# Performance work log

Measured on AMD Instinct MI355X. Metric: run time of the kernel, lower is better.

Reference implementation:

```python
import jax, jax.numpy as jnp
import numpy as np

B, S, D, H = 4, 1024, 1024, 16
HD = D // H          # head space dim = 64
FF = 4 * D           # ffn hidden = 4096
EPS = 1e-6

# ---- Lorentz manifold helpers (curvature k=1: -t^2 + |s|^2 = -1) ----

def to_manifold(space):
    t = jnp.sqrt(jnp.sum(space * space, -1, keepdims=True) + 1.0)
    return jnp.concatenate([t, space], -1)

def l_inner(x, y):
    return -x[..., 0] * y[..., 0] + jnp.sum(x[..., 1:] * y[..., 1:], -1)

def project(z):
    # renormalize onto hyperboloid: z / sqrt(|<z,z>_L|)   (Lorentz midpoint / LResNet)
    d = jnp.sqrt(jnp.clip(-l_inner(z, z), EPS))
    return z / d[..., None]

def hyp_layernorm(x, g, b):
    s = x[..., 1:]
    mu = jnp.mean(s, -1, keepdims=True)
    var = jnp.var(s, -1, keepdims=True)
    s = (s - mu) * jax.lax.rsqrt(var + 1e-5) * g + b
    return to_manifold(s)

def apply_rope(xs, cos, sin):
    # xs [B,S,H,HD]; cos/sin [S,HD//2]; freqs broadcast as [1,S,1,HD//2]
    x2 = xs.reshape(*xs.shape[:-1], HD // 2, 2)
    c = cos[None, :, None, :]
    s = sin[None, :, None, :]
    xr = x2[..., 0] * c - x2[..., 1] * s
    xi = x2[..., 0] * s + x2[..., 1] * c
    return jnp.stack([xr, xi], -1).reshape(xs.shape)


def setup_inputs() -> dict:
    key = jax.random.key(0)
    ks = jax.random.split(key, 8)
    def w(k, shape, fan_in):
        return jax.random.normal(k, shape, jnp.float32) / np.sqrt(fan_in).astype(np.float32)
    x = to_manifold(0.5 * jax.random.normal(ks[0], (B, S, D), jnp.float32))
    pos = jnp.arange(S, dtype=jnp.float32)[:, None]
    inv = 1.0 / (10000.0 ** (jnp.arange(0, HD, 2, dtype=jnp.float32) / HD))
    ang = pos * inv[None, :]
    return {
        'x': x,
        'rope_cos': jnp.cos(ang), 'rope_sin': jnp.sin(ang),
        'norm1_g': jnp.ones((D,), jnp.float32), 'norm1_b': jnp.zeros((D,), jnp.float32),
        'Wq': w(ks[1], (H, D + 1, HD), D + 1), 'bq': jnp.zeros((H, HD), jnp.float32),
        'Wk': w(ks[2], (H, D + 1, HD), D + 1), 'bk': jnp.zeros((H, HD), jnp.float32),
        'Wv': w(ks[3], (H, D + 1, HD), D + 1), 'bv': jnp.zeros((H, HD), jnp.float32),
        'attn_scale': jnp.asarray(np.sqrt(HD), jnp.float32),
        'attn_bias': jnp.zeros((), jnp.float32),
        'Wo': w(ks[4], (H * (HD + 1), D), H * (HD + 1)), 'bo': jnp.zeros((D,), jnp.float32),
        'w_res1': jnp.asarray(1.0, jnp.float32),
        'norm2_g': jnp.ones((D,), jnp.float32), 'norm2_b': jnp.zeros((D,), jnp.float32),
        'W1': w(ks[5], (D + 1, FF), D + 1), 'b1': jnp.zeros((FF,), jnp.float32),
        'W2': w(ks[6], (FF + 1, D), FF + 1), 'b2': jnp.zeros((D,), jnp.float32),
        'w_res2': jnp.asarray(1.0, jnp.float32),
    }


def reference(x, rope_cos, rope_sin, norm1_g, norm1_b, Wq, bq, Wk, bk, Wv, bv,
              attn_scale, attn_bias, Wo, bo, w_res1, norm2_g, norm2_b,
              W1, b1, W2, b2, w_res2):
    # ---- pre-norm ----
    xn = hyp_layernorm(x, norm1_g, norm1_b)
    # ---- per-head Lorentz linear (space part), inline RoPE on q/k ----
    qs = jnp.einsum('bsd,hde->bshe', xn, Wq) + bq          # [B,S,H,HD]
    ksp = jnp.einsum('bsd,hde->bshe', xn, Wk) + bk
    vsp = jnp.einsum('bsd,hde->bshe', xn, Wv) + bv
    qs = apply_rope(qs, rope_cos, rope_sin)
    ksp = apply_rope(ksp, rope_cos, rope_sin)
    # hyperbolic normalization of q/k: unit space norm, time recomputed
    qs = qs * jax.lax.rsqrt(jnp.sum(qs * qs, -1, keepdims=True) + EPS)
    ksp = ksp * jax.lax.rsqrt(jnp.sum(ksp * ksp, -1, keepdims=True) + EPS)
    q = to_manifold(qs)                                    # [B,S,H,HD+1]
    k = to_manifold(ksp)
    v = to_manifold(vsp)
    # ---- curvature-aware scores: 2 + 2 <q,k>_L (neg sq Lorentz distance) ----
    sgn = jnp.concatenate([-jnp.ones((1,), q.dtype), jnp.ones((HD,), q.dtype)])
    cin = jnp.einsum('bshe,bthe->bhst', q * sgn, k)        # Minkowski inner [B,H,S,S]
    att = (2.0 + 2.0 * cin) / attn_scale + attn_bias
    P = jax.nn.softmax(att, axis=-1)
    # ---- Lorentz midpoint aggregation of values ----
    m = jnp.einsum('bhst,bthe->bshe', P, v)
    m = project(m)                                         # back onto hyperboloid
    # ---- heads concat + output Lorentz linear ----
    cat = m.reshape(B, S, H * (HD + 1))
    attn_out = to_manifold(cat @ Wo + bo)
    # ---- LResNet residual 1 ----
    x = project(x + w_res1 * attn_out)
    # ---- Lorentz FFN ----
    h = hyp_layernorm(x, norm2_g, norm2_b)
    h = to_manifold(jax.nn.gelu(h @ W1 + b1))
    mlp = to_manifold(h @ W2 + b2)
    # ---- LResNet residual 2 ----
    x = project(x + w_res2 * mlp)
    return x
```

## Files before the change

### kernel.cpp

```cpp
#include <hip/hip_runtime.h>
#include <hip/hip_bf16.h>

typedef __hip_bfloat16 bf16;
typedef __attribute__((ext_vector_type(8))) short short8;
typedef __attribute__((ext_vector_type(4))) float f32x4;

#define B_  4
#define S_  1024
#define H_  16
#define R_  4096
#define LD_ 1088

#define MBL 1048576L
#define OFF_WQKVT (0L)
#define OFF_WOT   (6684672L)
#define OFF_X2    (0L)
#define OFF_W1T   (9L*MBL)
#define OFF_W2T   (18L*MBL)
#define OFF_BIAS  (26L*MBL)
#define OFF_XNB   (27L*MBL + MBL/2)
#define OFF_MCAT  OFF_XNB
#define OFF_HBUF  OFF_XNB
#define OFF_QPS   (36L*MBL)
#define OFF_ARAW  OFF_QPS
#define OFF_KPS   (44L*MBL)
#define OFF_VT    (52L*MBL)
#define OFF_QT    (62L*MBL)
#define OFF_KT    (62L*MBL + 262144L)
#define OFF_HHBIG (44L*MBL)
#define OFF_MLPB  (76L*MBL)
#define OFF_HHC   (36L*MBL)
#define OFF_MLPF  (44L*MBL)
#define BQKV 0
#define BOF  16384
#define B1F  32768
#define B2F  65536
#define W2R0 81920
#define RCF  98304
#define RSNF 262144
#define SCLF 409600
#define TACC 425984
#define FLAG 458752

__device__ __forceinline__ bf16  f2bf(float v) { return __float2bfloat16(v); }
__device__ __forceinline__ float bf2f(bf16 v)  { return __bfloat162float(v); }
__device__ __forceinline__ unsigned short bf2s(float v) {
  return __builtin_bit_cast(unsigned short, __float2bfloat16(v));
}
__device__ __forceinline__ float ldu(const void* p, long i, int isbf) {
  return isbf ? bf2f(((const bf16*)p)[i]) : ((const float*)p)[i];
}
__device__ __forceinline__ void stu(void* p, long i, float v, int isbf) {
  if (isbf) ((bf16*)p)[i] = f2bf(v);
  else      ((float*)p)[i] = v;
}
__device__ __forceinline__ float gelu_f(float v) {
  const float u = 0.7978845608028654f * (v + 0.044715f * v * v * v);
  const float e = __expf(fminf(2.f * u, 80.f));
  return 0.5f * v * (1.f + (e - 1.f) / (e + 1.f));
}
__device__ __forceinline__ float bfu_lo(unsigned u) {
  return __builtin_bit_cast(float, u << 16);
}
__device__ __forceinline__ float bfu_hi(unsigned u) {
  return __builtin_bit_cast(float, u & 0xFFFF0000u);
}

__device__ __forceinline__ void gload16(const bf16* g, short* l) {
  __builtin_amdgcn_global_load_lds(
      (const __attribute__((address_space(1))) unsigned int*)g,
      (__attribute__((address_space(3))) unsigned int*)l, 16, 0, 0);
}

__global__ void detect_kernel(const unsigned* __restrict__ g, int* __restrict__ flag) {
  if (threadIdx.x == 0) flag[0] = (g[0] == 0x3F803F80u) ? 1 : 0;
}

__global__ __launch_bounds__(256) void zero16_kernel(uint4* __restrict__ p, int n16) {
  int i = blockIdx.x * 256 + threadIdx.x;
  if (i < n16) p[i] = uint4{0, 0, 0, 0};
}

__device__ __forceinline__ float bred_f(float v, float* sh) {
#pragma unroll
  for (int o = 32; o; o >>= 1) v += __shfl_xor(v, o);
  __syncthreads();
  if ((threadIdx.x & 63) == 0) sh[threadIdx.x >> 6] = v;
  __syncthreads();
  return sh[0] + sh[1] + sh[2] + sh[3];
}
__device__ __forceinline__ double bred_d(double v, double* sh) {
#pragma unroll
  for (int o = 32; o; o >>= 1) v += __shfl_xor(v, o);
  __syncthreads();
  if ((threadIdx.x & 63) == 0) sh[threadIdx.x >> 6] = v;
  __syncthreads();
  return sh[0] + sh[1] + sh[2] + sh[3];
}

__global__ __launch_bounds__(256) void mega_prep(
    const void* x, const void* rc, const void* rsn, const void* n1g, const void* n1b,
    const void* Wq, const void* bq, const void* Wk, const void* bk,
    const void* Wv, const void* bv, const void* scl, const void* ab,
    const void* Wo, const void* bo, const void* wr1,
    const void* W1, const void* b1, const void* W2, const void* b2, const void* wr2,
    char* bias_base, bf16* __restrict__ wqkvT, bf16* __restrict__ woT,
    bf16* __restrict__ w1T, bf16* __restrict__ w2T, bf16* __restrict__ xnb,
    const int* __restrict__ flag) {
  const int isbf = flag[0];
  __shared__ float tl[64][65];
  const int tid = threadIdx.x;
  int bid = blockIdx.x;
  if (bid < 297) {
    int i = bid * 256 + tid;
    float* bqkvf = (float*)(bias_base + BQKV);
    if (i < 1024)        { bqkvf[i] = ldu(bq, i, isbf); return; }
    if (i < 2048)        { bqkvf[i] = ldu(bk, i - 1024, isbf); return; }
    if (i < 3072)        { bqkvf[i] = ldu(bv, i - 2048, isbf); return; }
    if (i < 4096)        { ((float*)(bias_base + BOF))[i - 3072] = ldu(bo, i - 3072, isbf); return; }
    if (i < 8192)        { ((float*)(bias_base + B1F))[i - 4096] = ldu(b1, i - 4096, isbf); return; }
    if (i < 9216)        { ((float*)(bias_base + B2F))[i - 8192] = ldu(b2, i - 8192, isbf); return; }
    if (i < 10240)       { ((float*)(bias_base + W2R0))[i - 9216] = ldu(W2, i - 9216, isbf); return; }
    if (i < 10240+32768) { ((float*)(bias_base + RCF))[i - 10240] = ldu(rc, i - 10240, isbf); return; }
    if (i < 10240+65536) { ((float*)(bias_base + RSNF))[i - 43008] = ldu(rsn, i - 43008, isbf); return; }
    if (i == 75776)      { ((float*)(bias_base + SCLF))[0] = ldu(scl, 0, isbf); return; }
    if (i == 75777)      { ((float*)(bias_base + SCLF))[1] = ldu(ab, 0, isbf); return; }
    if (i == 75778)      { ((float*)(bias_base + SCLF))[2] = ldu(wr1, 0, isbf); return; }
    if (i == 75779)      { ((float*)(bias_base + SCLF))[3] = ldu(wr2, 0, isbf); return; }
    return;
  }
  bid -= 297;
  const int tx = tid & 63, tg = tid >> 6;
  if (bid < 816) {
    int k0 = (bid % 17) * 64, z = bid / 17;
    int mode = z >> 4, h = z & 15;
    const void* src = (mode == 0) ? Wq : (mode == 1) ? Wk : Wv;
    const long soff = (long)h * 1025 * 64;
    int base_n = mode * 1024 + h * 64;
    for (int i = tg; i < 64; i += 4) {
      int k = k0 + i;
      tl[i][tx] = (k < 1025) ? ldu(src, soff + (long)k * 64 + tx, isbf) : 0.f;
    }
    __syncthreads();
    for (int i = tg; i < 64; i += 4) {
      int k = k0 + tx;
      if (k < LD_) wqkvT[(long)(base_n + i) * LD_ + k] = f2bf(tl[tx][i]);
    }
    return;
  }
  bid -= 816;
  if (bid < 272) {
    int k0 = (bid % 17) * 64, n0 = (bid / 17) * 64;
    for (int i = tg; i < 64; i += 4) {
      int kp = k0 + i;
      float v = 0.f;
      if (kp < 1056) {
        int h = kp / 66, e = kp - h * 66;
        if (e < 65) v = ldu(Wo, (long)(h * 65 + e) * 1024 + n0 + tx, isbf);
      }
      tl[i][tx] = v;
    }
    __syncthreads();
    for (int i = tg; i < 64; i += 4) {
      int kp = k0 + tx;
      if (kp < LD_) woT[(long)(n0 + i) * LD_ + kp] = f2bf(tl[tx][i]);
    }
    return;
  }
  bid -= 272;
  if (bid < 1088) {
    int k0 = (bid % 17) * 64, n0 = (bid / 17) * 64;
    for (int i = tg; i < 64; i += 4) {
      int k = k0 + i;
      tl[i][tx] = (k < 1025) ? ldu(W1, (long)k * 4096 + n0 + tx, isbf) : 0.f;
    }
    __syncthreads();
    for (int i = tg; i < 64; i += 4) {
      int k = k0 + tx;
      if (k < LD_) w1T[(long)(n0 + i) * LD_ + k] = f2bf(tl[tx][i]);
    }
    return;
  }
  bid -= 1088;
  if (bid < 1024) {
    int k0 = (bid % 64) * 64, n0 = (bid / 64) * 64;
    for (int i = tg; i < 64; i += 4) {
      int k = k0 + i;
      tl[i][tx] = ldu(W2, 1024 + (long)k * 1024 + n0 + tx, isbf);
    }
    __syncthreads();
    for (int i = tg; i < 64; i += 4) {
      int k = k0 + tx;
      w2T[(long)(n0 + i) * 4096 + k] = f2bf(tl[tx][i]);
    }
    return;
  }
  bid -= 1024;
  {
    float* red = &tl[0][0];
    const long base = (long)bid * 1025;
    const long obase = (long)bid * LD_;
    float v[4];
#pragma unroll
    for (int i = 0; i < 4; i++) v[i] = ldu(x, base + 1 + tid * 4 + i, isbf);
    float s = 0.f, s2 = 0.f;
#pragma unroll
    for (int i = 0; i < 4; i++) { s += v[i]; s2 += v[i] * v[i]; }
    s  = bred_f(s,  red);
    s2 = bred_f(s2, red);
    const float mu  = s * (1.f / 1024.f);
    const float var = s2 * (1.f / 1024.f) - mu * mu;
    const float rs  = rsqrtf(var + 1e-5f);
    float n[4], ns = 0.f;
#pragma unroll
    for (int i = 0; i < 4; i++) {
      const int e = tid * 4 + i;
      n[i] = (v[i] - mu) * rs * ldu(n1g, e, isbf) + ldu(n1b, e, isbf);
      ns += n[i] * n[i];
    }
    ns = bred_f(ns, red);
    if (tid == 0) xnb[obase] = f2bf(sqrtf(ns + 1.f));
#pragma unroll
    for (int i = 0; i < 4; i++) xnb[obase + 1 + tid * 4 + i] = f2bf(n[i]);
    if (tid < 63) xnb[obase + 1025 + tid] = f2bf(0.f);
  }
}

template <int EPI, bool SS>
__global__ __launch_bounds__(256) void mfma_gemm(const bf16* __restrict__ A, int lda,
                                                 const bf16* __restrict__ Bw, int ldb, int K,
                                                 const float* __restrict__ bias,
                                                 void* __restrict__ Cv, int ldc, int accf,
                                                 float* __restrict__ tacc) {
  __shared__ __align__(16) short As[2][128 * 32];
  __shared__ __align__(16) short Bs[2][64 * 32];
  const int tid = threadIdx.x, lane = tid & 63, wv = tid >> 6;
  const int quad = lane >> 4, q15 = lane & 15;
  const int wave_m = wv & 1, wave_n = wv >> 1;
  const int n0 = blockIdx.x * 64, m0 = blockIdx.y * 128;
  const int sa0 = wv * 128 + lane, sa1 = sa0 + 64;
  const int ra0 = sa0 >> 2, ca0 = (sa0 & 3) ^ (ra0 & 3);
  const int ra1 = sa1 >> 2, ca1 = (sa1 & 3) ^ (ra1 & 3);
  const int rb = tid >> 2, cb = (tid & 3) ^ (rb & 3);
  const int kswz = (quad ^ (q15 & 3)) * 8;
  const bf16* pa0 = A + (long)(m0 + ra0) * lda + ca0 * 8;
  const bf16* pa1 = A + (long)(m0 + ra1) * lda + ca1 * 8;
  const bf16* pb  = Bw + (long)(n0 + rb) * ldb + cb * 8;
  f32x4 acc[4][2] = {};
  for (int k0 = 0; k0 < K; k0 += 64) {
#pragma unroll
    for (int p = 0; p < 2; p++) {
      gload16(pa0 + p * 32, As[p] + sa0 * 8);
      gload16(pa1 + p * 32, As[p] + sa1 * 8);
      gload16(pb + p * 32, Bs[p] + tid * 8);
    }
    pa0 += 64; pa1 += 64; pb += 64;
    __syncthreads();
#pragma unroll
    for (int p = 0; p < 2; p++) {
      short8 af[4], bfr[2];
#pragma unroll
      for (int i = 0; i < 4; i++)
        af[i] = *(const short8*)(As[p] + (wave_m * 64 + i * 16 + q15) * 32 + kswz);
#pragma unroll
      for (int i = 0; i < 2; i++)
        bfr[i] = *(const short8*)(Bs[p] + (wave_n * 32 + i * 16 + q15) * 32 + kswz);
#pragma unroll
      for (int mi = 0; mi < 4; mi++)
#pragma unroll
        for (int ni = 0; ni < 2; ni++)
          acc[mi][ni] = __builtin_amdgcn_mfma_f32_16x16x32_bf16(af[mi], bfr[ni], acc[mi][ni], 0, 0, 0);
    }
    __syncthreads();
  }
#pragma unroll
  for (int mi = 0; mi < 4; mi++) {
#pragma unroll
    for (int r = 0; r < 4; r++) {
      const int m = m0 + wave_m * 64 + mi * 16 + quad * 4 + r;
      float s2 = 0.f;
#pragma unroll
      for (int ni = 0; ni < 2; ni++) {
        const int n = n0 + wave_n * 32 + ni * 16 + q15;
        float v = acc[mi][ni][r] + (bias ? bias[n] : 0.f);
        const long idx = (long)m * ldc + n;
        if (EPI == 0) {
          float* Cf = (float*)Cv;
          if (accf) v += Cf[idx];
          Cf[idx] = v;
        } else if (EPI == 1) {
          ((bf16*)Cv)[idx] = f2bf(v);
        } else {
          v = gelu_f(v);
          ((bf16*)Cv)[idx] = f2bf(v);
        }
        if (SS) s2 += v * v;
      }
      if (SS) {
        s2 += __shfl_xor(s2, 1);
        s2 += __shfl_xor(s2, 2);
        s2 += __shfl_xor(s2, 4);
        s2 += __shfl_xor(s2, 8);
        if (q15 == 0) atomicAdd(tacc + m, s2);
      }
    }
  }
}

template <int EPI>
__global__ __launch_bounds__(256) void mfma_gemm128(const bf16* __restrict__ A, int lda,
                                                    const bf16* __restrict__ Bw, int ldb, int K,
                                                    const float* __restrict__ bias,
                                                    void* __restrict__ Cv, int ldc, int accf) {
  __shared__ __align__(16) short As[2][128 * 32];
  __shared__ __align__(16) short Bs[2][128 * 32];
  const int tid = threadIdx.x, lane = tid & 63, wv = tid >> 6;
  const int quad = lane >> 4, q15 = lane & 15;
  const int wave_m = wv & 1, wave_n = wv >> 1;
  const int n0 = blockIdx.x * 128, m0 = blockIdx.y * 128;
  const int s0 = wv * 128 + lane, s1 = s0 + 64;
  const int r0 = s0 >> 2, c0 = (s0 & 3) ^ (r0 & 3);
  const int r1 = s1 >> 2, c1 = (s1 & 3) ^ (r1 & 3);
  const int kswz = (quad ^ (q15 & 3)) * 8;
  const bf16* pa0 = A + (long)(m0 + r0) * lda + c0 * 8;
  const bf16* pa1 = A + (long)(m0 + r1) * lda + c1 * 8;
  const bf16* pb0 = Bw + (long)(n0 + r0) * ldb + c0 * 8;
  const bf16* pb1 = Bw + (long)(n0 + r1) * ldb + c1 * 8;
  f32x4 acc[4][4] = {};
  for (int k0 = 0; k0 < K; k0 += 64) {
#pragma unroll
    for (int p = 0; p < 2; p++) {
      gload16(pa0 + p * 32, As[p] + s0 * 8);
      gload16(pa1 + p * 32, As[p] + s1 * 8);
      gload16(pb0 + p * 32, Bs[p] + s0 * 8);
      gload16(pb1 + p * 32, Bs[p] + s1 * 8);
    }
    pa0 += 64; pa1 += 64; pb0 += 64; pb1 += 64;
    __syncthreads();
#pragma unroll
    for (int p = 0; p < 2; p++) {
      short8 af[4], bfr[4];
#pragma unroll
      for (int i = 0; i < 4; i++) {
        af[i]  = *(const short8*)(As[p] + (wave_m * 64 + i * 16 + q15) * 32 + kswz);
        bfr[i] = *(const short8*)(Bs[p] + (wave_n * 64 + i * 16 + q15) * 32 + kswz);
      }
#pragma unroll
      for (int mi = 0; mi < 4; mi++)
#pragma unroll
        for (int ni = 0; ni < 4; ni++)
          acc[mi][ni] = __builtin_amdgcn_mfma_f32_16x16x32_bf16(af[mi], bfr[ni], acc[mi][ni], 0, 0, 0);
    }
    __syncthreads();
  }
#pragma unroll
  for (int mi = 0; mi < 4; mi++) {
#pragma unroll
    for (int r = 0; r < 4; r++) {
      const int m = m0 + wave_m * 64 + mi * 16 + quad * 4 + r;
#pragma unroll
      for (int ni = 0; ni < 4; ni++) {
        const int n = n0 + wave_n * 64 + ni * 16 + q15;
        float v = acc[mi][ni][r] + (bias ? bias[n] : 0.f);
        const long idx = (long)m * ldc + n;
        if (EPI == 0) {
          float* Cf = (float*)Cv;
          if (accf) v += Cf[idx];
          Cf[idx] = v;
        } else if (EPI == 1) {
          ((bf16*)Cv)[idx] = f2bf(v);
        } else {
          ((bf16*)Cv)[idx] = f2bf(gelu_f(v));
        }
      }
    }
  }
}

__global__ __launch_bounds__(256) void gemm_qkv(const bf16* __restrict__ A,
                                                const bf16* __restrict__ Wt,
                                                const char* __restrict__ bias_base,
                                                bf16* __restrict__ qPs, float* __restrict__ qtc,
                                                bf16* __restrict__ kPs, float* __restrict__ ktc,
                                                bf16* __restrict__ vT) {
  __shared__ __align__(16) short As[2][128 * 32];
  __shared__ __align__(16) short Bs[2][128 * 32];
  const int tid = threadIdx.x, lane = tid & 63, wv = tid >> 6;
  const int quad = lane >> 4, q15 = lane & 15;
  const int wave_m = wv & 1, wave_n = wv >> 1;
  const int n0 = blockIdx.x * 128, m0 = blockIdx.y * 128;
  const int s0 = wv * 128 + lane, s1 = s0 + 64;
  const int r0 = s0 >> 2, c0 = (s0 & 3) ^ (r0 & 3);
  const int r1 = s1 >> 2, c1 = (s1 & 3) ^ (r1 & 3);
  const int kswz = (quad ^ (q15 & 3)) * 8;
  const float* bqkvf = (const float*)(bias_base + BQKV);
  const float* rcf   = (const float*)(bias_base + RCF);
  const float* rsnf  = (const float*)(bias_base + RSNF);
  const bf16* pa0 = A + (long)(m0 + r0) * LD_ + c0 * 8;
  const bf16* pa1 = A + (long)(m0 + r1) * LD_ + c1 * 8;
  const bf16* pb0 = Wt + (long)(n0 + r0) * LD_ + c0 * 8;
  const bf16* pb1 = Wt + (long)(n0 + r1) * LD_ + c1 * 8;
  f32x4 acc[4][4] = {};
  for (int k0 = 0; k0 < LD_; k0 += 64) {
#pragma unroll
    for (int p = 0; p < 2; p++) {
      gload16(pa0 + p * 32, As[p] + s0 * 8);
      gload16(pa1 + p * 32, As[p] + s1 * 8);
      gload16(pb0 + p * 32, Bs[p] + s0 * 8);
      gload16(pb1 + p * 32, Bs[p] + s1 * 8);
    }
    pa0 += 64; pa1 += 64; pb0 += 64; pb1 += 64;
    __syncthreads();
#pragma unroll
    for (int p = 0; p < 2; p++) {
      short8 af[4], bfr[4];
#pragma unroll
      for (int i = 0; i < 4; i++) {
        af[i]  = *(const short8*)(As[p] + (wave_m * 64 + i * 16 + q15) * 32 + kswz);
        bfr[i] = *(const short8*)(Bs[p] + (wave_n * 64 + i * 16 + q15) * 32 + kswz);
      }
#pragma unroll
      for (int mi = 0; mi < 4; mi++)
#pragma unroll
        for (int ni = 0; ni < 4; ni++)
          acc[mi][ni] = __builtin_amdgcn_mfma_f32_16x16x32_bf16(af[mi], bfr[ni], acc[mi][ni], 0, 0, 0);
    }
    __syncthreads();
  }
  const int hg = (n0 >> 6) + wave_n;
  const int mode = hg >> 4, h = hg & 15;
  const int nb = hg * 64;
#pragma unroll
  for (int mi = 0; mi < 4; mi++) {
#pragma unroll
    for (int r = 0; r < 4; r++) {
      const int m = m0 + wave_m * 64 + mi * 16 + quad * 4 + r;
      const int bb = m >> 10, s = m & 1023;
      const int bh = bb * H_ + h;
      float v[4];
#pragma unroll
      for (int ns = 0; ns < 4; ns++) v[ns] = acc[mi][ns][r] + bqkvf[nb + ns * 16 + q15];
      if (mode < 2) {
#pragma unroll
        for (int ns = 0; ns < 4; ns++) {
          const int eg = ns * 16 + q15;
          const int j = eg >> 1;
          const float c = rcf[s * 32 + j], sn = rsnf[s * 32 + j];
          const float p = __shfl_xor(v[ns], 1);
          v[ns] = ((eg & 1) == 0) ? (v[ns] * c - p * sn) : (p * sn + v[ns] * c);
        }
      }
      float ss = v[0] * v[0] + v[1] * v[1] + v[2] * v[2] + v[3] * v[3];
#pragma unroll
      for (int o = 8; o; o >>= 1) ss += __shfl_xor(ss, o);
      if (mode == 0) {
        const float sc = rsqrtf(ss + 1e-6f);
        const long rb2 = (long)(bh * 1024 + s) * 64;
#pragma unroll
        for (int ns = 0; ns < 4; ns++) qPs[rb2 + ns * 16 + q15] = f2bf(v[ns] * sc);
        if (q15 == 0) qtc[bh * 1024 + s] = sqrtf(ss / (ss + 1e-6f) + 1.f);
      } else if (mode == 1) {
        const float sc = rsqrtf(ss + 1e-6f);
        const long rb2 = (long)(bh * 1024 + s) * 64;
#pragma unroll
        for (int ns = 0; ns < 4; ns++) kPs[rb2 + ns * 16 + q15] = f2bf(v[ns] * sc);
        if (q15 == 0) ktc[bh * 1024 + s] = sqrtf(ss / (ss + 1e-6f) + 1.f);
      } else {
        const long vb = (long)bh * 81920;
#pragma unroll
        for (int ns = 0; ns < 4; ns++) vT[vb + (long)(1 + ns * 16 + q15) * 1024 + s] = f2bf(v[ns]);
        if (q15 == 0) vT[vb + s] = f2bf(sqrtf(ss + 1.f));
      }
    }
  }
}

__global__ __launch_bounds__(256) void attn_kernel(const bf16* __restrict__ qPs,
                                                   const float* __restrict__ qtc,
                                                   const bf16* __restrict__ kPs,
                                                   const float* __restrict__ ktc,
                                                   const bf16* __restrict__ vT,
                                                   const float* __restrict__ scalf,
                                                   bf16* __restrict__ mcat) {
  __shared__ __align__(16) short kbuf[64 * 72];
  __shared__ __align__(16) short vbuf[80 * 72];
  __shared__ __align__(16) short pbuf[64 * 72];
  __shared__ float tkl[64];
  const int tid = threadIdx.x, lane = tid & 63, wv = tid >> 6;
  const int quad = lane >> 4, q15 = lane & 15;
  const int id = blockIdx.x;
  const int cxd = id & 7, jj_ = id >> 3;
  const int bh = cxd * 8 + (jj_ & 7), qt_ = jj_ >> 3;
  const float inv_scale = 1.f / scalf[0];
  const long qrow = (long)(bh * 1024 + qt_ * 64 + wv * 16 + q15) * 64;
  const short8 aq0 = *(const short8*)(qPs + qrow + quad * 8);
  const short8 aq1 = *(const short8*)(qPs + qrow + 32 + quad * 8);
  float tqr[4];
#pragma unroll
  for (int r = 0; r < 4; r++) tqr[r] = qtc[bh * 1024 + qt_ * 64 + wv * 16 + quad * 4 + r];
  f32x4 out[5];
#pragma unroll
  for (int mt = 0; mt < 5; mt++) out[mt] = f32x4{0, 0, 0, 0};
  float lip[4] = {0.f, 0.f, 0.f, 0.f};
  const int srcl = (q15 >> 2) << 4;
  for (int kt = 0; kt < 16; kt++) {
    __syncthreads();
#pragma unroll
    for (int c = 0; c < 2; c++) {
      const int id2 = c * 256 + tid, row = id2 >> 3, off = id2 & 7;
      *(uint4*)(kbuf + row * 72 + off * 8) =
          *(const uint4*)(kPs + (long)(bh * 1024 + kt * 64 + row) * 64 + off * 8);
    }
#pragma unroll
    for (int c = 0; c < 3; c++) {
      const int id2 = c * 256 + tid;
      if (id2 < 640) {
        const int row = id2 >> 3, off = id2 & 7;
        *(uint4*)(vbuf + row * 72 + off * 8) =
            *(const uint4*)(vT + (long)bh * 81920 + (long)row * 1024 + kt * 64 + off * 8);
      }
    }
    if (tid < 64) tkl[tid] = ktc[bh * 1024 + kt * 64 + tid];
    __syncthreads();
    f32x4 sacc[4] = {f32x4{0,0,0,0}, f32x4{0,0,0,0}, f32x4{0,0,0,0}, f32x4{0,0,0,0}};
#pragma unroll
    for (int ns = 0; ns < 4; ns++) {
      short8 b0 = *(const short8*)(kbuf + (ns * 16 + q15) * 72 + quad * 8);
      short8 b1 = *(const short8*)(kbuf + (ns * 16 + q15) * 72 + 32 + quad * 8);
      sacc[ns] = __builtin_amdgcn_mfma_f32_16x16x32_bf16(aq0, b0, sacc[ns], 0, 0, 0);
      sacc[ns] = __builtin_amdgcn_mfma_f32_16x16x32_bf16(aq1, b1, sacc[ns], 0, 0, 0);
    }
#pragma unroll
    for (int ns = 0; ns < 4; ns++) {
      const float tk = tkl[ns * 16 + q15];
#pragma unroll
      for (int r = 0; r < 4; r++) {
        const float pv = __expf((2.f + 2.f * (sacc[ns][r] - tqr[r] * tk)) * inv_scale);
        lip[r] += pv;
        pbuf[(wv * 16 + quad * 4 + r) * 72 + ns * 16 + q15] = (short)bf2s(pv);
      }
    }
#pragma unroll
    for (int mt = 0; mt < 5; mt++)
#pragma unroll
      for (int kc = 0; kc < 2; kc++) {
        short8 av = *(const short8*)(vbuf + (mt * 16 + q15) * 72 + kc * 32 + quad * 8);
        short8 bp = *(const short8*)(pbuf + (wv * 16 + q15) * 72 + kc * 32 + quad * 8);
        out[mt] = __builtin_amdgcn_mfma_f32_16x16x32_bf16(av, bp, out[mt], 0, 0, 0);
      }
  }
  {
#pragma unroll
    for (int o = 8; o; o >>= 1)
#pragma unroll
      for (int r = 0; r < 4; r++) lip[r] += __shfl_xor(lip[r], o);
    float linv[4];
#pragma unroll
    for (int r = 0; r < 4; r++) linv[r] = 1.f / lip[r];
    const float t0 = __shfl(linv[0], srcl), t1 = __shfl(linv[1], srcl);
    const float t2 = __shfl(linv[2], srcl), t3 = __shfl(linv[3], srcl);
    const int rr = q15 & 3;
    const float lv = (rr == 0) ? t0 : (rr == 1) ? t1 : (rr == 2) ? t2 : t3;
#pragma unroll
    for (int mt = 0; mt < 5; mt++)
#pragma unroll
      for (int j = 0; j < 4; j++) out[mt][j] *= lv;
  }
  float part = 0.f;
#pragma unroll
  for (int mt = 0; mt < 5; mt++)
#pragma unroll
    for (int j = 0; j < 4; j++) {
      const int e = mt * 16 + quad * 4 + j;
      const float vv = out[mt][j] * out[mt][j];
      part += (e == 0) ? vv : -vv;
    }
  part += __shfl_xor(part, 16);
  part += __shfl_xor(part, 32);
  const float dinv = rsqrtf(fmaxf(part, 1e-6f));
  __syncthreads();
  short* obuf = vbuf;
  const int qrow_l = wv * 16 + q15;
#pragma unroll
  for (int mt = 0; mt < 5; mt++)
#pragma unroll
    for (int j = 0; j < 4; j++) {
      const int e = mt * 16 + quad * 4 + j;
      if (e <= 64) obuf[qrow_l * 72 + e] = (short)bf2s(out[mt][j] * dinv);
    }
  if (quad == 1) obuf[qrow_l * 72 + 65] = 0;
  __syncthreads();
  const int b = bh >> 4, h = bh & 15;
  const long outbase = ((long)b * 1024 + qt_ * 64) * LD_ + h * 66;
  for (int i = tid; i < 64 * 33; i += 256) {
    const int row = i / 33, p = i - row * 33;
    *(unsigned*)(mcat + outbase + (long)row * LD_ + p * 2) =
        *(const unsigned*)(obuf + row * 72 + p * 2);
  }
  if (h == 15) {
    const long zb = ((long)b * 1024 + qt_ * 64) * LD_ + 1056;
    for (int i = tid; i < 64 * 16; i += 256) {
      const int row = i >> 4, p = i & 15;
      *(unsigned*)(mcat + zb + (long)row * LD_ + p * 2) = 0u;
    }
  }
}

__global__ __launch_bounds__(256) void final_fix_kernel(const float* __restrict__ t_acc,
                                                        const float* __restrict__ w2r0,
                                                        const float* __restrict__ b2f,
                                                        float* __restrict__ mlp) {
  const int m = blockIdx.x;
  const float t = sqrtf(1.f + t_acc[m]);
  float* row = mlp + (long)m * 1024;
  for (int n = threadIdx.x; n < 1024; n += 256) row[n] += t * w2r0[n] + b2f[n];
}

__global__ __launch_bounds__(256) void final_fix_big(const bf16* __restrict__ hh,
                                                     const float* __restrict__ w2r0,
                                                     const float* __restrict__ b2f,
                                                     float* __restrict__ mlp) {
  __shared__ float red[4];
  const int m = blockIdx.x;
  const uint4* r4 = (const uint4*)(hh + (long)m * 4096);
  float ss = 0.f;
  for (int i = threadIdx.x; i < 512; i += 256) {
    const uint4 u = r4[i];
    const unsigned a[4] = {u.x, u.y, u.z, u.w};
#pragma unroll
    for (int j = 0; j < 4; j++) {
      const float lo = bfu_lo(a[j]), hi = bfu_hi(a[j]);
      ss += lo * lo + hi * hi;
    }
  }
  ss = bred_f(ss, red);
  const float t = sqrtf(1.f + ss);
  float* row = mlp + (long)m * 1024;
  for (int n = threadIdx.x; n < 1024; n += 256) row[n] += t * w2r0[n] + b2f[n];
}

__global__ __launch_bounds__(256) void proj_ln_kernel(
    const void* __restrict__ x, const bf16* __restrict__ c,
    const float* __restrict__ scalf, int widx,
    const void* __restrict__ g, const void* __restrict__ b,
    bf16* __restrict__ x2, bf16* __restrict__ hbuf, const int* __restrict__ flag) {
  const int isbf = flag[0];
  __shared__ double redd[4];
  __shared__ float redf[4];
  const long bx = (long)blockIdx.x * 1025;
  const long bc = (long)blockIdx.x * 1024;
  const long ob = (long)blockIdx.x * LD_;
  const int tid = threadIdx.x;
  const double w = (double)scalf[widx];
  const float x0 = ldu(x, bx, isbf);
  float xs[4], cv[4];
#pragma unroll
  for (int i = 0; i < 4; i++) {
    xs[i] = ldu(x, bx + 1 + tid * 4 + i, isbf);
    cv[i] = bf2f(c[bc + tid * 4 + i]);
  }
  double cc = 0.0, xx = 0.0, xc = 0.0, sx = 0.0, sc_ = 0.0;
#pragma unroll
  for (int i = 0; i < 4; i++) {
    cc += (double)cv[i] * cv[i];
    xx += (double)xs[i] * xs[i];
    xc += (double)xs[i] * cv[i];
    sx += (double)xs[i];
    sc_ += (double)cv[i];
  }
  cc = bred_d(cc, redd);
  xx = bred_d(xx, redd);
  xc = bred_d(xc, redd);
  sx = bred_d(sx, redd);
  sc_ = bred_d(sc_, redd);
  const double t   = sqrt(1.0 + cc);
  const double lxx = (double)x0 * x0 - xx;
  const double xm  = -(double)x0 * t + xc;
  double d2 = lxx + w * w - 2.0 * w * xm;
  if (d2 < 1e-6) d2 = 1e-6;
  const double dinv = 1.0 / sqrt(d2);
  if (tid == 0) x2[bx] = f2bf((float)(((double)x0 + w * t) * dinv));
  float z[4];
#pragma unroll
  for (int i = 0; i < 4; i++) {
    z[i] = (float)(((double)xs[i] + w * cv[i]) * dinv);
    x2[bx + 1 + tid * 4 + i] = f2bf(z[i]);
  }
  const float sumz  = (float)((sx + w * sc_) * dinv);
  const float sumsq = (float)((xx + 2.0 * w * xc + w * w * cc) * dinv * dinv);
  const float mu  = sumz * (1.f / 1024.f);
  const float var = sumsq * (1.f / 1024.f) - mu * mu;
  const float rs  = rsqrtf(var + 1e-5f);
  float n[4], ns = 0.f;
#pragma unroll
  for (int i = 0; i < 4; i++) {
    const int e = tid * 4 + i;
    n[i] = (z[i] - mu) * rs * ldu(g, e, isbf) + ldu(b, e, isbf);
    ns += n[i] * n[i];
  }
  ns = bred_f(ns, redf);
  if (tid == 0) hbuf[ob] = f2bf(sqrtf(ns + 1.f));
#pragma unroll
  for (int i = 0; i < 4; i++) hbuf[ob + 1 + tid * 4 + i] = f2bf(n[i]);
  if (tid < 63) hbuf[ob + 1025 + tid] = f2bf(0.f);
}

__global__ __launch_bounds__(256) void res_project_kernel(
    const void* __restrict__ x, int xtag, const void* __restrict__ c, int ctag,
    const float* __restrict__ scalf, int widx, void* __restrict__ out, int otag,
    const int* __restrict__ flag) {
  const int isbf = flag[0];
  const int xb = (xtag == 2) ? isbf : xtag;
  const int cb2 = (ctag == 2) ? isbf : ctag;
  const int ob = (otag == 2) ? isbf : otag;
  __shared__ double red[4];
  const long bx = (long)blockIdx.x * 1025;
  const long bc = (long)blockIdx.x * 1024;
  const int tid = threadIdx.x;
  const double w = (double)scalf[widx];
  const float x0 = ldu(x, bx, xb);
  float xs[4], cv[4];
#pragma unroll
  for (int i = 0; i < 4; i++) {
    xs[i] = ldu(x, bx + 1 + tid * 4 + i, xb);
    cv[i] = ldu(c, bc + tid * 4 + i, cb2);
  }
  double cc = 0.0, xx = 0.0, xc = 0.0;
#pragma unroll
  for (int i = 0; i < 4; i++) {
    cc += (double)cv[i] * cv[i];
    xx += (double)xs[i] * xs[i];
    xc += (double)xs[i] * cv[i];
  }
  cc = bred_d(cc, red);
  xx = bred_d(xx, red);
  xc = bred_d(xc, red);
  const double t   = sqrt(1.0 + cc);
  const double lxx = (double)x0 * x0 - xx;
  const double xm  = -(double)x0 * t + xc;
  double d2 = lxx + w * w - 2.0 * w * xm;
  if (d2 < 1e-6) d2 = 1e-6;
  const double dinv = 1.0 / sqrt(d2);
  if (tid == 0) stu(out, bx, (float)(((double)x0 + w * t) * dinv), ob);
#pragma unroll
  for (int i = 0; i < 4; i++)
    stu(out, bx + 1 + tid * 4 + i, (float)(((double)xs[i] + w * cv[i]) * dinv), ob);
}

extern "C" void kernel_launch(void* const* d_in, const int* in_sizes, int n_in,
                              void* d_out, int out_size, void* d_ws, size_t ws_size,
                              hipStream_t stream) {
  char* w = (char*)d_ws;
  char* bias_base = w + OFF_BIAS;
  int* flag = (int*)(bias_base + FLAG);
  float* tacc = (float*)(bias_base + TACC);
  const float* scalf = (const float*)(bias_base + SCLF);
  const bool big = ws_size >= (size_t)92 * MBL;
  char* mlp_off = big ? (w + OFF_MLPB) : (w + OFF_MLPF);

  detect_kernel<<<1, 64, 0, stream>>>((const unsigned*)d_in[3], flag);
  zero16_kernel<<<4, 256, 0, stream>>>((uint4*)tacc, 1024);

  mega_prep<<<7593, 256, 0, stream>>>(
      d_in[0], d_in[1], d_in[2], d_in[3], d_in[4], d_in[5], d_in[6], d_in[7], d_in[8],
      d_in[9], d_in[10], d_in[11], d_in[12], d_in[13], d_in[14], d_in[15], d_in[18],
      d_in[19], d_in[20], d_in[21], d_in[22], bias_base, (bf16*)(w + OFF_WQKVT),
      (bf16*)(w + OFF_WOT), (bf16*)(w + OFF_W1T), (bf16*)(w + OFF_W2T),
      (bf16*)(w + OFF_XNB), flag);

  gemm_qkv<<<dim3(24, 32), 256, 0, stream>>>(
      (const bf16*)(w + OFF_XNB), (const bf16*)(w + OFF_WQKVT), bias_base,
      (bf16*)(w + OFF_QPS), (float*)(w + OFF_QT), (bf16*)(w + OFF_KPS),
      (float*)(w + OFF_KT), (bf16*)(w + OFF_VT));
  attn_kernel<<<1024, 256, 0, stream>>>(
      (const bf16*)(w + OFF_QPS), (const float*)(w + OFF_QT), (const bf16*)(w + OFF_KPS),
      (const float*)(w + OFF_KT), (const bf16*)(w + OFF_VT), scalf, (bf16*)(w + OFF_MCAT));
  mfma_gemm<1, false><<<dim3(16, 32), 256, 0, stream>>>(
      (const bf16*)(w + OFF_MCAT), LD_, (const bf16*)(w + OFF_WOT), LD_, LD_,
      (const float*)(bias_base + BOF), w + OFF_ARAW, 1024, 0, nullptr);
  proj_ln_kernel<<<R_, 256, 0, stream>>>(d_in[0], (const bf16*)(w + OFF_ARAW), scalf, 2,
                                         d_in[16], d_in[17], (bf16*)(w + OFF_X2),
                                         (bf16*)(w + OFF_HBUF), flag);
  if (big) {
    mfma_gemm128<2><<<dim3(32, 32), 256, 0, stream>>>(
        (const bf16*)(w + OFF_HBUF), LD_, (const bf16*)(w + OFF_W1T), LD_, LD_,
        (const float*)(bias_base + B1F), w + OFF_HHBIG, 4096, 0);
    mfma_gemm<0, false><<<dim3(16, 32), 256, 0, stream>>>(
        (const bf16*)(w + OFF_HHBIG), 4096, (const bf16*)(w + OFF_W2T), 4096, 4096,
        nullptr, mlp_off, 1024, 0, nullptr);
    final_fix_big<<<R_, 256, 0, stream>>>((const bf16*)(w + OFF_HHBIG),
                                          (const float*)(bias_base + W2R0),
                                          (const float*)(bias_base + B2F),
                                          (float*)mlp_off);
  } else {
    for (int c = 0; c < 4; c++) {
      mfma_gemm<2, true><<<dim3(16, 32), 256, 0, stream>>>(
          (const bf16*)(w + OFF_HBUF), LD_, (const bf16*)(w + OFF_W1T) + (long)c * 1024 * LD_,
          LD_, LD_, (const float*)(bias_base + B1F) + c * 1024, w + OFF_HHC, 1024, 0, tacc);
      mfma_gemm<0, false><<<dim3(16, 32), 256, 0, stream>>>(
          (const bf16*)(w + OFF_HHC), 1024, (const bf16*)(w + OFF_W2T) + c * 1024, 4096, 1024,
          nullptr, mlp_off, 1024, c > 0 ? 1 : 0, nullptr);
    }
    final_fix_kernel<<<R_, 256, 0, stream>>>(tacc, (const float*)(bias_base + W2R0),
                                             (const float*)(bias_base + B2F),
                                             (float*)mlp_off);
  }
  res_project_kernel<<<R_, 256, 0, stream>>>(w + OFF_X2, 1, mlp_off, 0, scalf, 3,
                                             d_out, 2, flag);
}
```

Measured before the change: 470.4 us.

## Use 128x64 tiles with XCD swizzle and split-K for FFN down GEMM

Replaces the 128x128-tile QKV and FFN-up GEMMs with 128x64 tiles, doubling the grid. The QKV epilogue now reduces per-row sums of squares across waves through shared memory. Adds an XCD-aware block remap to the generic GEMM, and splits the FFN-down GEMM (K=4096) into two K halves via blockIdx.z, with the second partial summed in final_fix_big. The aim is more blocks in flight and better L2 locality across chiplets, at the cost of less reuse per tile, an extra fp32 partial buffer, and a shared-memory sync in the QKV epilogue.

Result: slower. 486.3 us (+3.4%).

```diff
diff --git a/kernel.cpp b/kernel.cpp
--- a/kernel.cpp
+++ b/kernel.cpp
@@ -21,6 +21,7 @@
 #define OFF_XNB   (27L*MBL + MBL/2)
 #define OFF_MCAT  OFF_XNB
 #define OFF_HBUF  OFF_XNB
+#define OFF_PART1 OFF_XNB
 #define OFF_QPS   (36L*MBL)
 #define OFF_ARAW  OFF_QPS
 #define OFF_KPS   (44L*MBL)
@@ -70,6 +71,20 @@
   __builtin_amdgcn_global_load_lds(
       (const __attribute__((address_space(1))) unsigned int*)g,
       (__attribute__((address_space(3))) unsigned int*)l, 16, 0, 0);
+}
+
+__device__ __forceinline__ void xcd_swz(int& bx, int& by) {
+  const int nbx = gridDim.x;
+  const int nb = nbx * gridDim.y;
+  if ((nb & 7) == 0) {
+    const int hid = blockIdx.y * nbx + blockIdx.x;
+    const int l = (hid & 7) * (nb >> 3) + (hid >> 3);
+    bx = l % nbx;
+    by = l / nbx;
+  } else {
+    bx = blockIdx.x;
+    by = blockIdx.y;
+  }
 }
 
 __global__ void detect_kernel(const unsigned* __restrict__ g, int* __restrict__ flag) {
@@ -231,21 +246,25 @@
                                                  const bf16* __restrict__ Bw, int ldb, int K,
                                                  const float* __restrict__ bias,
                                                  void* __restrict__ Cv, int ldc, int accf,
-                                                 float* __restrict__ tacc) {
+                                                 float* __restrict__ tacc,
+                                                 int kz, float* __restrict__ Cz1) {
   __shared__ __align__(16) short As[2][128 * 32];
   __shared__ __align__(16) short Bs[2][64 * 32];
   const int tid = threadIdx.x, lane = tid & 63, wv = tid >> 6;
   const int quad = lane >> 4, q15 = lane & 15;
   const int wave_m = wv & 1, wave_n = wv >> 1;
-  const int n0 = blockIdx.x * 64, m0 = blockIdx.y * 128;
+  int bx, by;
+  xcd_swz(bx, by);
+  const int n0 = bx * 64, m0 = by * 128;
+  const long zoff = (long)blockIdx.z * kz;
   const int sa0 = wv * 128 + lane, sa1 = sa0 + 64;
   const int ra0 = sa0 >> 2, ca0 = (sa0 & 3) ^ (ra0 & 3);
   const int ra1 = sa1 >> 2, ca1 = (sa1 & 3) ^ (ra1 & 3);
   const int rb = tid >> 2, cb = (tid & 3) ^ (rb & 3);
   const int kswz = (quad ^ (q15 & 3)) * 8;
-  const bf16* pa0 = A + (long)(m0 + ra0) * lda + ca0 * 8;
-  const bf16* pa1 = A + (long)(m0 + ra1) * lda + ca1 * 8;
-  const bf16* pb  = Bw + (long)(n0 + rb) * ldb + cb * 8;
+  const bf16* pa0 = A + zoff + (long)(m0 + ra0) * lda + ca0 * 8;
+  const bf16* pa1 = A + zoff + (long)(m0 + ra1) * lda + ca1 * 8;
+  const bf16* pb  = Bw + zoff + (long)(n0 + rb) * ldb + cb * 8;
   f32x4 acc[4][2] = {};
   for (int k0 = 0; k0 < K; k0 += 64) {
 #pragma unroll
@@ -285,7 +304,7 @@
         float v = acc[mi][ni][r] + (bias ? bias[n] : 0.f);
         const long idx = (long)m * ldc + n;
         if (EPI == 0) {
-          float* Cf = (float*)Cv;
+          float* Cf = (blockIdx.z && Cz1) ? Cz1 : (float*)Cv;
           if (accf) v += Cf[idx];
           Cf[idx] = v;
         } else if (EPI == 1) {
@@ -307,169 +326,127 @@
   }
 }
 
-template <int EPI>
-__global__ __launch_bounds__(256) void mfma_gemm128(const bf16* __restrict__ A, int lda,
-                                                    const bf16* __restrict__ Bw, int ldb, int K,
-                                                    const float* __restrict__ bias,
-                                                    void* __restrict__ Cv, int ldc, int accf) {
+__global__ __launch_bounds__(256) void gemm_qkv128(const bf16* __restrict__ A,
+                                                   const bf16* __restrict__ Wt,
+                                                   const char* __restrict__ bias_base,
+                                                   bf16* __restrict__ qPs, float* __restrict__ qtc,
+                                                   bf16* __restrict__ kPs, float* __restrict__ ktc,
+                                                   bf16* __restrict__ vT) {
   __shared__ __align__(16) short As[2][128 * 32];
-  __shared__ __align__(16) short Bs[2][128 * 32];
+  __shared__ __align__(16) short Bs[2][64 * 32];
+  __shared__ float sred[2][128];
   const int tid = threadIdx.x, lane = tid & 63, wv = tid >> 6;
   const int quad = lane >> 4, q15 = lane & 15;
   const int wave_m = wv & 1, wave_n = wv >> 1;
-  const int n0 = blockIdx.x * 128, m0 = blockIdx.y * 128;
-  const int s0 = wv * 128 + lane, s1 = s0 + 64;
-  const int r0 = s0 >> 2, c0 = (s0 & 3) ^ (r0 & 3);
-  const int r1 = s1 >> 2, c1 = (s1 & 3) ^ (r1 & 3);
+  int bx, by;
+  xcd_swz(bx, by);
+  const int n0 = bx * 64, m0 = by * 128;
+  const int sa0 = wv * 128 + lane, sa1 = sa0 + 64;
+  const int ra0 = sa0 >> 2, ca0 = (sa0 & 3) ^ (ra0 & 3);
+  const int ra1 = sa1 >> 2, ca1 = (sa1 & 3) ^ (ra1 & 3);
+  const int rb = tid >> 2, cb = (tid & 3) ^ (rb & 3);
   const int kswz = (quad ^ (q15 & 3)) * 8;
-  const bf16* pa0 = A + (long)(m0 + r0) * lda + c0 * 8;
-  const bf16* pa1 = A + (long)(m0 + r1) * lda + c1 * 8;
-  const bf16* pb0 = Bw + (long)(n0 + r0) * ldb + c0 * 8;
-  const bf16* pb1 = Bw + (long)(n0 + r1) * ldb + c1 * 8;
-  f32x4 acc[4][4] = {};
-  for (int k0 = 0; k0 < K; k0 += 64) {
+  const bf16* pa0 = A + (long)(m0 + ra0) * LD_ + ca0 * 8;
+  const bf16* pa1 = A + (long)(m0 + ra1) * LD_ + ca1 * 8;
+  const bf16* pb  = Wt + (long)(n0 + rb) * LD_ + cb * 8;
+  f32x4 acc[4][2] = {};
+  for (int k0 = 0; k0 < LD_; k0 += 64) {
 #pragma unroll
     for (int p = 0; p < 2; p++) {
-      gload16(pa0 + p * 32, As[p] + s0 * 8);
-      gload16(pa1 + p * 32, As[p] + s1 * 8);
-      gload16(pb0 + p * 32, Bs[p] + s0 * 8);
-      gload16(pb1 + p * 32, Bs[p] + s1 * 8);
-    }
-    pa0 += 64; pa1 += 64; pb0 += 64; pb1 += 64;
+      gload16(pa0 + p * 32, As[p] + sa0 * 8);
+      gload16(pa1 + p * 32, As[p] + sa1 * 8);
+      gload16(pb + p * 32, Bs[p] + tid * 8);
+    }
+    pa0 += 64; pa1 += 64; pb += 64;
     __syncthreads();
 #pragma unroll
     for (int p = 0; p < 2; p++) {
-      short8 af[4], bfr[4];
-#pragma unroll
-      for (int i = 0; i < 4; i++) {
-        af[i]  = *(const short8*)(As[p] + (wave_m * 64 + i * 16 + q15) * 32 + kswz);
-        bfr[i] = *(const short8*)(Bs[p] + (wave_n * 64 + i * 16 + q15) * 32 + kswz);
-      }
+      short8 af[4], bfr[2];
+#pragma unroll
+      for (int i = 0; i < 4; i++)
+        af[i] = *(const short8*)(As[p] + (wave_m * 64 + i * 16 + q15) * 32 + kswz);
+#pragma unroll
+      for (int i = 0; i < 2; i++)
+        bfr[i] = *(const short8*)(Bs[p] + (wave_n * 32 + i * 16 + q15) * 32 + kswz);
 #pragma unroll
       for (int mi = 0; mi < 4; mi++)
 #pragma unroll
-        for (int ni = 0; ni < 4; ni++)
+        for (int ni = 0; ni < 2; ni++)
           acc[mi][ni] = __builtin_amdgcn_mfma_f32_16x16x32_bf16(af[mi], bfr[ni], acc[mi][ni], 0, 0, 0);
     }
     __syncthreads();
   }
-#pragma unroll
-  for (int mi = 0; mi < 4; mi++) {
-#pragma unroll
-    for (int r = 0; r < 4; r++) {
-      const int m = m0 + wave_m * 64 + mi * 16 + quad * 4 + r;
-#pragma unroll
-      for (int ni = 0; ni < 4; ni++) {
-        const int n = n0 + wave_n * 64 + ni * 16 + q15;
-        float v = acc[mi][ni][r] + (bias ? bias[n] : 0.f);
-        const long idx = (long)m * ldc + n;
-        if (EPI == 0) {
-          float* Cf = (float*)Cv;
-          if (accf) v += Cf[idx];
-          Cf[idx] = v;
-        } else if (EPI == 1) {
-          ((bf16*)Cv)[idx] = f2bf(v);
-        } else {
-          ((bf16*)Cv)[idx] = f2bf(gelu_f(v));
-        }
-      }
-    }
-  }
-}
-
-__global__ __launch_bounds__(256) void gemm_qkv(const bf16* __restrict__ A,
-                                                const bf16* __restrict__ Wt,
-                                                const char* __restrict__ bias_base,
-                                                bf16* __restrict__ qPs, float* __restrict__ qtc,
-                                                bf16* __restrict__ kPs, float* __restrict__ ktc,
-                                                bf16* __restrict__ vT) {
-  __shared__ __align__(16) short As[2][128 * 32];
-  __shared__ __align__(16) short Bs[2][128 * 32];
-  const int tid = threadIdx.x, lane = tid & 63, wv = tid >> 6;
-  const int quad = lane >> 4, q15 = lane & 15;
-  const int wave_m = wv & 1, wave_n = wv >> 1;
-  const int n0 = blockIdx.x * 128, m0 = blockIdx.y * 128;
-  const int s0 = wv * 128 + lane, s1 = s0 + 64;
-  const int r0 = s0 >> 2, c0 = (s0 & 3) ^ (r0 & 3);
-  const int r1 = s1 >> 2, c1 = (s1 & 3) ^ (r1 & 3);
-  const int kswz = (quad ^ (q15 & 3)) * 8;
   const float* bqkvf = (const float*)(bias_base + BQKV);
   const float* rcf   = (const float*)(bias_base + RCF);
   const float* rsnf  = (const float*)(bias_base + RSNF);
-  const bf16* pa0 = A + (long)(m0 + r0) * LD_ + c0 * 8;
-  const bf16* pa1 = A + (long)(m0 + r1) * LD_ + c1 * 8;
-  const bf16* pb0 = Wt + (long)(n0 + r0) * LD_ + c0 * 8;
-  const bf16* pb1 = Wt + (long)(n0 + r1) * LD_ + c1 * 8;
-  f32x4 acc[4][4] = {};
-  for (int k0 = 0; k0 < LD_; k0 += 64) {
-#pragma unroll
-    for (int p = 0; p < 2; p++) {
-      gload16(pa0 + p * 32, As[p] + s0 * 8);
-      gload16(pa1 + p * 32, As[p] + s1 * 8);
-      gload16(pb0 + p * 32, Bs[p] + s0 * 8);
-      gload16(pb1 + p * 32, Bs[p] + s1 * 8);
-    }
-    pa0 += 64; pa1 += 64; pb0 += 64; pb1 += 64;
-    __syncthreads();
-#pragma unroll
-    for (int p = 0; p < 2; p++) {
-      short8 af[4], bfr[4];
-#pragma unroll
-      for (int i = 0; i < 4; i++) {
-        af[i]  = *(const short8*)(As[p] + (wave_m * 64 + i * 16 + q15) * 32 + kswz);
-        bfr[i] = *(const short8*)(Bs[p] + (wave_n * 64 + i * 16 + q15) * 32 + kswz);
-      }
-#pragma unroll
-      for (int mi = 0; mi < 4; mi++)
-#pragma unroll
-        for (int ni = 0; ni < 4; ni++)
-          acc[mi][ni] = __builtin_amdgcn_mfma_f32_16x16x32_bf16(af[mi], bfr[ni], acc[mi][ni], 0, 0, 0);
-    }
-    __syncthreads();
-  }
-  const int hg = (n0 >> 6) + wave_n;
+  const int hg = bx;
   const int mode = hg >> 4, h = hg & 15;
-  const int nb = hg * 64;
+  float ssp[4][4];
 #pragma unroll
   for (int mi = 0; mi < 4; mi++) {
 #pragma unroll
     for (int r = 0; r < 4; r++) {
       const int m = m0 + wave_m * 64 + mi * 16 + quad * 4 + r;
+      const int s = m & 1023;
+      float v0 = acc[mi][0][r] + bqkvf[hg * 64 + wave_n * 32 + q15];
+      float v1 = acc[mi][1][r] + bqkvf[hg * 64 + wave_n * 32 + 16 + q15];
+      if (mode < 2) {
+        {
+          const int eg = wave_n * 32 + q15;
+          const int j = eg >> 1;
+          const float c = rcf[s * 32 + j], sn = rsnf[s * 32 + j];
+          const float p = __shfl_xor(v0, 1);
+          v0 = ((eg & 1) == 0) ? (v0 * c - p * sn) : (p * sn + v0 * c);
+        }
+        {
+          const int eg = wave_n * 32 + 16 + q15;
+          const int j = eg >> 1;
+          const float c = rcf[s * 32 + j], sn = rsnf[s * 32 + j];
+          const float p = __shfl_xor(v1, 1);
+          v1 = ((eg & 1) == 0) ? (v1 * c - p * sn) : (p * sn + v1 * c);
+        }
+      }
+      acc[mi][0][r] = v0;
+      acc[mi][1][r] = v1;
+      float ss = v0 * v0 + v1 * v1;
+#pragma unroll
+      for (int o = 8; o; o >>= 1) ss += __shfl_xor(ss, o);
+      ssp[mi][r] = ss;
+    }
+  }
+#pragma unroll
+  for (int mi = 0; mi < 4; mi++)
+#pragma unroll
+    for (int r = 0; r < 4; r++)
+      if (q15 == 0) sred[wave_n][wave_m * 64 + mi * 16 + quad * 4 + r] = ssp[mi][r];
+  __syncthreads();
+#pragma unroll
+  for (int mi = 0; mi < 4; mi++) {
+#pragma unroll
+    for (int r = 0; r < 4; r++) {
+      const int wrow = wave_m * 64 + mi * 16 + quad * 4 + r;
+      const float sst = sred[0][wrow] + sred[1][wrow];
+      const int m = m0 + wrow;
       const int bb = m >> 10, s = m & 1023;
       const int bh = bb * H_ + h;
-      float v[4];
-#pragma unroll
-      for (int ns = 0; ns < 4; ns++) v[ns] = acc[mi][ns][r] + bqkvf[nb + ns * 16 + q15];
-      if (mode < 2) {
-#pragma unroll
-        for (int ns = 0; ns < 4; ns++) {
-          const int eg = ns * 16 + q15;
-          const int j = eg >> 1;
-          const float c = rcf[s * 32 + j], sn = rsnf[s * 32 + j];
-          const float p = __shfl_xor(v[ns], 1);
-          v[ns] = ((eg & 1) == 0) ? (v[ns] * c - p * sn) : (p * sn + v[ns] * c);
-        }
-      }
-      float ss = v[0] * v[0] + v[1] * v[1] + v[2] * v[2] + v[3] * v[3];
-#pragma unroll
-      for (int o = 8; o; o >>= 1) ss += __shfl_xor(ss, o);
+      const float v0 = acc[mi][0][r], v1 = acc[mi][1][r];
       if (mode == 0) {
-        const float sc = rsqrtf(ss + 1e-6f);
+        const float sc = rsqrtf(sst + 1e-6f);
         const long rb2 = (long)(bh * 1024 + s) * 64;
-#pragma unroll
-        for (int ns = 0; ns < 4; ns++) qPs[rb2 + ns * 16 + q15] = f2bf(v[ns] * sc);
-        if (q15 == 0) qtc[bh * 1024 + s] = sqrtf(ss / (ss + 1e-6f) + 1.f);
+        qPs[rb2 + wave_n * 32 + q15] = f2bf(v0 * sc);
+        qPs[rb2 + wave_n * 32 + 16 + q15] = f2bf(v1 * sc);
+        if (wave_n == 0 && q15 == 0) qtc[bh * 1024 + s] = sqrtf(sst / (sst + 1e-6f) + 1.f);
       } else if (mode == 1) {
-        const float sc = rsqrtf(ss + 1e-6f);
+        const float sc = rsqrtf(sst + 1e-6f);
         const long rb2 = (long)(bh * 1024 + s) * 64;
-#pragma unroll
-        for (int ns = 0; ns < 4; ns++) kPs[rb2 + ns * 16 + q15] = f2bf(v[ns] * sc);
-        if (q15 == 0) ktc[bh * 1024 + s] = sqrtf(ss / (ss + 1e-6f) + 1.f);
+        kPs[rb2 + wave_n * 32 + q15] = f2bf(v0 * sc);
+        kPs[rb2 + wave_n * 32 + 16 + q15] = f2bf(v1 * sc);
+        if (wave_n == 0 && q15 == 0) ktc[bh * 1024 + s] = sqrtf(sst / (sst + 1e-6f) + 1.f);
       } else {
         const long vb = (long)bh * 81920;
-#pragma unroll
-        for (int ns = 0; ns < 4; ns++) vT[vb + (long)(1 + ns * 16 + q15) * 1024 + s] = f2bf(v[ns]);
-        if (q15 == 0) vT[vb + s] = f2bf(sqrtf(ss + 1.f));
+        vT[vb + (long)(1 + wave_n * 32 + q15) * 1024 + s] = f2bf(v0);
+        vT[vb + (long)(1 + wave_n * 32 + 16 + q15) * 1024 + s] = f2bf(v1);
+        if (wave_n == 0 && q15 == 0) vT[vb + s] = f2bf(sqrtf(sst + 1.f));
       }
     }
   }
@@ -619,6 +596,7 @@
 __global__ __launch_bounds__(256) void final_fix_big(const bf16* __restrict__ hh,
                                                      const float* __restrict__ w2r0,
                                                      const float* __restrict__ b2f,
+                                                     const float* __restrict__ part1,
                                                      float* __restrict__ mlp) {
   __shared__ float red[4];
   const int m = blockIdx.x;
@@ -636,7 +614,9 @@
   ss = bred_f(ss, red);
   const float t = sqrtf(1.f + ss);
   float* row = mlp + (long)m * 1024;
-  for (int n = threadIdx.x; n < 1024; n += 256) row[n] += t * w2r0[n] + b2f[n];
+  const float* prow = part1 + (long)m * 1024;
+  for (int n = threadIdx.x; n < 1024; n += 256)
+    row[n] += prow[n] + t * w2r0[n] + b2f[n];
 }
 
 __global__ __launch_bounds__(256) void proj_ln_kernel(
@@ -768,7 +748,7 @@
       (bf16*)(w + OFF_WOT), (bf16*)(w + OFF_W1T), (bf16*)(w + OFF_W2T),
       (bf16*)(w + OFF_XNB), flag);
 
-  gemm_qkv<<<dim3(24, 32), 256, 0, stream>>>(
+  gemm_qkv128<<<dim3(48, 32), 256, 0, stream>>>(
       (const bf16*)(w + OFF_XNB), (const bf16*)(w + OFF_WQKVT), bias_base,
       (bf16*)(w + OFF_QPS), (float*)(w + OFF_QT), (bf16*)(w + OFF_KPS),
       (float*)(w + OFF_KT), (bf16*)(w + OFF_VT));
@@ -777,29 +757,31 @@
       (const float*)(w + OFF_KT), (const bf16*)(w + OFF_VT), scalf, (bf16*)(w + OFF_MCAT));
   mfma_gemm<1, false><<<dim3(16, 32), 256, 0, stream>>>(
       (const bf16*)(w + OFF_MCAT), LD_, (const bf16*)(w + OFF_WOT), LD_, LD_,
-      (const float*)(bias_base + BOF), w + OFF_ARAW, 1024, 0, nullptr);
+      (const float*)(bias_base + BOF), w + OFF_ARAW, 1024, 0, nullptr, 0, nullptr);
   proj_ln_kernel<<<R_, 256, 0, stream>>>(d_in[0], (const bf16*)(w + OFF_ARAW), scalf, 2,
                                          d_in[16], d_in[17], (bf16*)(w + OFF_X2),
                                          (bf16*)(w + OFF_HBUF), flag);
   if (big) {
-    mfma_gemm128<2><<<dim3(32, 32), 256, 0, stream>>>(
+    mfma_gemm<2, false><<<dim3(64, 32), 256, 0, stream>>>(
         (const bf16*)(w + OFF_HBUF), LD_, (const bf16*)(w + OFF_W1T), LD_, LD_,
-        (const float*)(bias_base + B1F), w + OFF_HHBIG, 4096, 0);
-    mfma_gemm<0, false><<<dim3(16, 32), 256, 0, stream>>>(
-        (const bf16*)(w + OFF_HHBIG), 4096, (const bf16*)(w + OFF_W2T), 4096, 4096,
-        nullptr, mlp_off, 1024, 0, nullptr);
+        (const float*)(bias_base + B1F), w + OFF_HHBIG, 4096, 0, nullptr, 0, nullptr);
+    mfma_gemm<0, false><<<dim3(16, 32, 2), 256, 0, stream>>>(
+        (const bf16*)(w + OFF_HHBIG), 4096, (const bf16*)(w + OFF_W2T), 4096, 2048,
+        nullptr, mlp_off, 1024, 0, nullptr, 2048, (float*)(w + OFF_PART1));
     final_fix_big<<<R_, 256, 0, stream>>>((const bf16*)(w + OFF_HHBIG),
                                           (const float*)(bias_base + W2R0),
                                           (const float*)(bias_base + B2F),
+                                          (const float*)(w + OFF_PART1),
                                           (float*)mlp_off);
   } else {
     for (int c = 0; c < 4; c++) {
       mfma_gemm<2, true><<<dim3(16, 32), 256, 0, stream>>>(
           (const bf16*)(w + OFF_HBUF), LD_, (const bf16*)(w + OFF_W1T) + (long)c * 1024 * LD_,
-          LD_, LD_, (const float*)(bias_base + B1F) + c * 1024, w + OFF_HHC, 1024, 0, tacc);
+          LD_, LD_, (const float*)(bias_base + B1F) + c * 1024, w + OFF_HHC, 1024, 0, tacc,
+          0, nullptr);
       mfma_gemm<0, false><<<dim3(16, 32), 256, 0, stream>>>(
           (const bf16*)(w + OFF_HHC), 1024, (const bf16*)(w + OFF_W2T) + c * 1024, 4096, 1024,
-          nullptr, mlp_off, 1024, c > 0 ? 1 : 0, nullptr);
+          nullptr, mlp_off, 1024, c > 0 ? 1 : 0, nullptr, 0, nullptr);
     }
     final_fix_kernel<<<R_, 256, 0, stream>>>(tacc, (const float*)(bias_base + W2R0),
                                              (const float*)(bias_base + B2F),
```
